# Performance work log

Measured on AMD Instinct MI355X. Metric: run time of the kernel, lower is better.

Reference implementation:

```python
import jax, jax.numpy as jnp
import numpy as np

B, S, D = 16, 512, 768      # batch, max_n_words, context_dim (input_size)
E, R = 128, 2048            # entities per doc, candidate relations per doc
H = 768                     # config.hidden_size
H2 = H // 2                 # 384
OUT = 2                     # binary relation classes


def _linear_params(k, fan_in, fan_out):
    k1, k2 = jax.random.split(k)
    bound = 1.0 / np.sqrt(fan_in)
    W = jax.random.uniform(k1, (fan_in, fan_out), minval=-bound, maxval=bound, dtype=jnp.float32)
    b = jax.random.uniform(k2, (fan_out,), minval=-bound, maxval=bound, dtype=jnp.float32)
    return W, b


def setup_inputs() -> dict:
    key = jax.random.key(0)
    ks = jax.random.split(key, 16)
    hW1, hb1 = _linear_params(ks[0], 2 * D, H)
    hW2, hb2 = _linear_params(ks[1], H, H2)
    tW1, tb1 = _linear_params(ks[2], 2 * D, H)
    tW2, tb2 = _linear_params(ks[3], H, H2)
    bnd = 1.0 / np.sqrt(H2)
    bil_w = jax.random.uniform(ks[4], (OUT, H2, H2), minval=-bnd, maxval=bnd, dtype=jnp.float32)
    lW, lb = _linear_params(ks[5], 2 * H2, OUT)
    emb = jax.random.normal(ks[6], (3, D), dtype=jnp.float32)  # entity_emb
    hidden_states = jax.random.normal(ks[7], (B, S, D), dtype=jnp.float32)
    ent_start = jax.random.randint(ks[8], (B, E), 0, S)
    ent_label = jax.random.randint(ks[9], (B, E), 0, 3)
    rel_head = jax.random.randint(ks[10], (B, R), 0, E)
    rel_tail = jax.random.randint(ks[11], (B, R), 0, E)
    rel_label = jax.random.randint(ks[12], (B, R), 0, 2)
    return dict(hidden_states=hidden_states, emb=emb,
                hW1=hW1, hb1=hb1, hW2=hW2, hb2=hb2,
                tW1=tW1, tb1=tb1, tW2=tW2, tb2=tb2,
                bil_w=bil_w, lW=lW, lb=lb,
                ent_start=ent_start, ent_label=ent_label,
                rel_head=rel_head, rel_tail=rel_tail, rel_label=rel_label)


def reference(hidden_states, emb, hW1, hb1, hW2, hb2, tW1, tb1, tW2, tb2,
              bil_w, lW, lb, ent_start, ent_label, rel_head, rel_tail, rel_label):
    def tower(rel_idx, W1, b1, W2, b2):
        start = jnp.take_along_axis(ent_start, rel_idx, axis=1)              # [B,R]
        lab = jnp.take_along_axis(ent_label, rel_idx, axis=1)                # [B,R]
        hid = jnp.take_along_axis(hidden_states, start[..., None], axis=1)   # [B,R,D]
        rep = jnp.concatenate([hid, emb[lab]], axis=-1)                      # [B,R,2D]
        h = jax.nn.relu(rep @ W1 + b1)                                       # [B,R,H]
        return jax.nn.relu(h @ W2 + b2)                                      # [B,R,H2]

    heads = tower(rel_head, hW1, hb1, hW2, hb2)
    tails = tower(rel_tail, tW1, tb1, tW2, tb2)
    # Biaffine: bilinear (no bias) + linear over concat
    logits = (jnp.einsum('bri,oij,brj->bro', heads, bil_w, tails)
              + jnp.concatenate([heads, tails], axis=-1) @ lW + lb)          # [B,R,2]
    logp = jax.nn.log_softmax(logits, axis=-1)
    loss = -jnp.mean(jnp.take_along_axis(logp, rel_label[..., None], axis=-1))
    return loss, logits
```

## Files before the change

### kernel.cpp

```cpp
#include <hip/hip_runtime.h>
#include <hip/hip_bf16.h>
#include <cstdint>

typedef unsigned short ushort_t;
typedef __bf16 bf16x8 __attribute__((ext_vector_type(8)));
typedef float f32x4 __attribute__((ext_vector_type(4)));

#define B_   16
#define S_   512
#define D_   768
#define E_   128
#define R_   2048
#define NREL 32768

__device__ inline ushort_t f2b(float f) {
    uint32_t u = __builtin_bit_cast(uint32_t, f);
    uint32_t r = (u + 0x7fffu + ((u >> 16) & 1u)) >> 16;
    return (ushort_t)r;
}
__device__ inline float b2f(ushort_t u) {
    uint32_t v = ((uint32_t)u) << 16;
    return __builtin_bit_cast(float, v);
}
__device__ inline float bl(uint32_t u) {
    uint32_t v = u << 16;
    return __builtin_bit_cast(float, v);
}
__device__ inline float bh(uint32_t u) {
    uint32_t v = u & 0xffff0000u;
    return __builtin_bit_cast(float, v);
}

__global__ __launch_bounds__(256) void prep_kernel(
    const float* __restrict__ hidden, const float* __restrict__ lW,
    const int* __restrict__ ent_start,
    ushort_t* __restrict__ repE, ushort_t* __restrict__ BmatT,
    ushort_t* __restrict__ lWtT, float* __restrict__ out)
{
    int idx = blockIdx.x * 256 + threadIdx.x;
    if (idx == 0) out[0] = 0.0f;
    if (idx < 393216) {
        int row = idx / 192, q = idx - row * 192;
        int c = q * 4;
        int b = row >> 7;
        int st = ent_start[row];
        const float* srcp = hidden + ((size_t)(b * S_ + st) * D_ + c);
        float4 v = *reinterpret_cast<const float4*>(srcp);
        uint32_t lo = (uint32_t)f2b(v.x) | ((uint32_t)f2b(v.y) << 16);
        uint32_t hi = (uint32_t)f2b(v.z) | ((uint32_t)f2b(v.w) << 16);
        uint2 pk; pk.x = lo; pk.y = hi;
        *reinterpret_cast<uint2*>(repE + (size_t)idx * 4) = pk;
        return;
    }
    int i2 = idx - 393216;
    if (i2 < 768) {
        int o = i2 / 384, kk = i2 - o * 384;
        BmatT[(768 + o) * 384 + kk] = f2b(lW[kk * 2 + o]);
        return;
    }
    i2 -= 768;
    if (i2 < 768) {
        int o = i2 / 384, ii = i2 - o * 384;
        lWtT[o * 384 + ii] = f2b(lW[(384 + ii) * 2 + o]);
    }
}

__global__ __launch_bounds__(256) void transpose_w(
    const float* __restrict__ hW1, const float* __restrict__ tW1,
    const float* __restrict__ hW2, const float* __restrict__ tW2,
    const float* __restrict__ bil, const float* __restrict__ emb,
    const float* __restrict__ hb1, const float* __restrict__ tb1,
    ushort_t* __restrict__ hW1T, ushort_t* __restrict__ tW1T,
    ushort_t* __restrict__ hW2T, ushort_t* __restrict__ tW2T,
    ushort_t* __restrict__ BmatT,
    float* __restrict__ biasEh, float* __restrict__ biasEt)
{
    __shared__ float smem[1056];
    int z = blockIdx.z;
    if (z >= 6) {
        if (blockIdx.y || blockIdx.x >= 12) return;
        const float* W1 = (z == 6) ? hW1 : tW1;
        const float* b1 = (z == 6) ? hb1 : tb1;
        float* dstB     = (z == 6) ? biasEh : biasEt;
        int c64 = threadIdx.x & 63, kc = threadIdx.x >> 6;
        int col = blockIdx.x * 64 + c64;
        float a0 = 0.f, a1 = 0.f, a2 = 0.f;
        const float* wp = W1 + (size_t)(768 + kc * 192) * 768 + col;
        const float* e0 = emb + kc * 192;
        for (int k = 0; k < 192; ++k) {
            float w = wp[(size_t)k * 768];
            a0 += e0[k] * w;
            a1 += e0[768 + k] * w;
            a2 += e0[1536 + k] * w;
        }
        smem[(kc * 3 + 0) * 64 + c64] = a0;
        smem[(kc * 3 + 1) * 64 + c64] = a1;
        smem[(kc * 3 + 2) * 64 + c64] = a2;
        __syncthreads();
        if (kc == 0) {
            float bv = b1[col];
#pragma unroll
            for (int l = 0; l < 3; ++l) {
                float s = smem[l * 64 + c64] + smem[(3 + l) * 64 + c64]
                        + smem[(6 + l) * 64 + c64] + smem[(9 + l) * 64 + c64];
                dstB[l * 768 + col] = bv + s;
            }
        }
        return;
    }
    const float* src; ushort_t* dst; int Rr, Cc;
    switch (z) {
        case 0:  src = hW1;          dst = hW1T;           Rr = 768; Cc = 768; break;
        case 1:  src = tW1;          dst = tW1T;           Rr = 768; Cc = 768; break;
        case 2:  src = hW2;          dst = hW2T;           Rr = 768; Cc = 384; break;
        case 3:  src = tW2;          dst = tW2T;           Rr = 768; Cc = 384; break;
        case 4:  src = bil;          dst = BmatT;          Rr = 384; Cc = 384; break;
        default: src = bil + 147456; dst = BmatT + 147456; Rr = 384; Cc = 384; break;
    }
    int tR = blockIdx.x * 32, tC = blockIdx.y * 32;
    if (tR >= Rr || tC >= Cc) return;
    int tx = threadIdx.x & 31, ty = threadIdx.x >> 5;
#pragma unroll
    for (int r = 0; r < 4; ++r)
        smem[(ty + r * 8) * 33 + tx] = src[(size_t)(tR + ty + r * 8) * Cc + tC + tx];
    __syncthreads();
#pragma unroll
    for (int r = 0; r < 4; ++r)
        dst[(size_t)(tC + ty + r * 8) * Rr + tR + tx] = f2b(smem[tx * 33 + ty + r * 8]);
}

__global__ __launch_bounds__(256) void gemm_lds(
    const ushort_t* __restrict__ A0, const ushort_t* __restrict__ A1,
    const ushort_t* __restrict__ Bt0, const ushort_t* __restrict__ Bt1,
    const float* __restrict__ bias0, const float* __restrict__ bias1,
    void* __restrict__ out0, void* __restrict__ out1,
    const int* __restrict__ lab,
    int M, int N0, int N1, int K, int doRelu, int f32o0, int f32o1)
{
    __shared__ ushort_t As[64 * 32];
    __shared__ ushort_t Bs[64 * 32];
    int N = blockIdx.z ? N1 : N0;
    int tileN = blockIdx.y * 64;
    if (tileN >= N) return;
    const ushort_t* A   = blockIdx.z ? A1 : A0;
    const ushort_t* Bt  = blockIdx.z ? Bt1 : Bt0;
    const float*   bias = blockIdx.z ? bias1 : bias0;
    int           f32o  = blockIdx.z ? f32o1 : f32o0;
    ushort_t*      outH = (ushort_t*)(blockIdx.z ? out1 : out0);
    float*         outF = (float*)(blockIdx.z ? out1 : out0);

    int t = threadIdx.x;
    int lane = t & 63, wave = t >> 6;
    int tileM = blockIdx.x * 64;
    int wm = (wave >> 1) * 32, wn = (wave & 1) * 32;
    int l15 = lane & 15, quad = lane >> 4;

    const ushort_t* gA = A  + (size_t)tileM * K;
    const ushort_t* gB = Bt + (size_t)tileN * K;

    int srow = t >> 2, sc8 = (t & 3) << 3;

    f32x4 acc[2][2];
#pragma unroll
    for (int a = 0; a < 2; ++a)
#pragma unroll
        for (int b = 0; b < 2; ++b) {
            acc[a][b][0] = 0.f; acc[a][b][1] = 0.f;
            acc[a][b][2] = 0.f; acc[a][b][3] = 0.f;
        }

    for (int k0 = 0; k0 < K; k0 += 32) {
        __builtin_amdgcn_global_load_lds(
            (const __attribute__((address_space(1))) void*)(gA + (size_t)srow * K + k0 + sc8),
            (__attribute__((address_space(3))) void*)(As + t * 8), 16, 0, 0);
        __builtin_amdgcn_global_load_lds(
            (const __attribute__((address_space(1))) void*)(gB + (size_t)srow * K + k0 + sc8),
            (__attribute__((address_space(3))) void*)(Bs + t * 8), 16, 0, 0);
        __syncthreads();
        bf16x8 af[2], bfr[2];
#pragma unroll
        for (int mi = 0; mi < 2; ++mi)
            af[mi] = *reinterpret_cast<const bf16x8*>(As + (wm + mi * 16 + l15) * 32 + quad * 8);
#pragma unroll
        for (int ni = 0; ni < 2; ++ni)
            bfr[ni] = *reinterpret_cast<const bf16x8*>(Bs + (wn + ni * 16 + l15) * 32 + quad * 8);
#pragma unroll
        for (int mi = 0; mi < 2; ++mi)
#pragma unroll
            for (int ni = 0; ni < 2; ++ni)
                acc[mi][ni] = __builtin_amdgcn_mfma_f32_16x16x32_bf16(af[mi], bfr[ni], acc[mi][ni], 0, 0, 0);
        __syncthreads();
    }

#pragma unroll
    for (int mi = 0; mi < 2; ++mi) {
        int gr = tileM + wm + mi * 16 + quad * 4;
        int lb4[4];
        if (lab) {
#pragma unroll
            for (int r = 0; r < 4; ++r) lb4[r] = lab[gr + r];
        }
#pragma unroll
        for (int ni = 0; ni < 2; ++ni) {
            int gc = tileN + wn + ni * 16 + l15;
            if (gc < N) {
#pragma unroll
                for (int r = 0; r < 4; ++r) {
                    float bb = lab ? bias[(size_t)lb4[r] * N + gc]
                                   : (bias ? bias[gc] : 0.0f);
                    float v = acc[mi][ni][r] + bb;
                    if (doRelu) v = fmaxf(v, 0.0f);
                    if (f32o) outF[(size_t)(gr + r) * N + gc] = v;
                    else      outH[(size_t)(gr + r) * N + gc] = f2b(v);
                }
            }
        }
    }
}

__global__ __launch_bounds__(256) void rel_kernel(
    const ushort_t* __restrict__ Uext, const ushort_t* __restrict__ tailsE,
    const float* __restrict__ tLin, const float* __restrict__ lb,
    const int* __restrict__ rel_head, const int* __restrict__ rel_tail,
    const int* __restrict__ rel_label, float* __restrict__ out)
{
    __shared__ float wsum[4];
    int lane = threadIdx.x & 63, wave = threadIdx.x >> 6;
    float lb0 = lb[0], lb1 = lb[1];
    float lossAcc = 0.0f;
    int base = (blockIdx.x * 4 + wave) * 8;

    for (int q = 0; q < 8; ++q) {
        int rel = base + q;
        int b = rel >> 11;
        int h = rel_head[rel], t = rel_tail[rel], lab = rel_label[rel];
        const uint32_t* uh = reinterpret_cast<const uint32_t*>(Uext + (size_t)(b * E_ + h) * 770);
        const uint32_t* tv = reinterpret_cast<const uint32_t*>(tailsE + (size_t)(b * E_ + t) * 384);

        float a0 = 0.f, a1 = 0.f;
#pragma unroll
        for (int j = 0; j < 3; ++j) {
            int i = lane + 64 * j;
            uint32_t tu = tv[i];
            uint32_t u0 = uh[i], u1 = uh[192 + i];
            float tl = bl(tu), th = bh(tu);
            a0 += tl * bl(u0) + th * bh(u0);
            a1 += tl * bl(u1) + th * bh(u1);
        }
#pragma unroll
        for (int d = 1; d < 64; d <<= 1) {
            a0 += __shfl_xor(a0, d);
            a1 += __shfl_xor(a1, d);
        }
        const ushort_t* uhs = reinterpret_cast<const ushort_t*>(uh);
        float2 tp = reinterpret_cast<const float2*>(tLin)[b * E_ + t];
        float l0v = a0 + tp.x + b2f(uhs[768]) + lb0;
        float l1v = a1 + tp.y + b2f(uhs[769]) + lb1;
        if (lane == 0) {
            out[1 + 2 * rel]     = l0v;
            out[1 + 2 * rel + 1] = l1v;
        }
        float m = fmaxf(l0v, l1v);
        float lse = m + logf(expf(l0v - m) + expf(l1v - m));
        lossAcc += lse - (lab ? l1v : l0v);
    }
    if (lane == 0) wsum[wave] = lossAcc;
    __syncthreads();
    if (threadIdx.x == 0) {
        float s = wsum[0] + wsum[1] + wsum[2] + wsum[3];
        atomicAdd(out, s * (1.0f / 32768.0f));
    }
}

extern "C" void kernel_launch(void* const* d_in, const int* in_sizes, int n_in,
                              void* d_out, int out_size, void* d_ws, size_t ws_size,
                              hipStream_t stream)
{
    const float* hidden = (const float*)d_in[0];
    const float* emb    = (const float*)d_in[1];
    const float* hW1    = (const float*)d_in[2];
    const float* hb1    = (const float*)d_in[3];
    const float* hW2    = (const float*)d_in[4];
    const float* hb2    = (const float*)d_in[5];
    const float* tW1    = (const float*)d_in[6];
    const float* tb1    = (const float*)d_in[7];
    const float* tW2    = (const float*)d_in[8];
    const float* tb2    = (const float*)d_in[9];
    const float* bil    = (const float*)d_in[10];
    const float* lW     = (const float*)d_in[11];
    const float* lb     = (const float*)d_in[12];
    const int* ent_start = (const int*)d_in[13];
    const int* ent_label = (const int*)d_in[14];
    const int* rel_head  = (const int*)d_in[15];
    const int* rel_tail  = (const int*)d_in[16];
    const int* rel_label = (const int*)d_in[17];
    float* out = (float*)d_out;

    char* ws = (char*)d_ws;
    ushort_t* repE   = (ushort_t*)(ws + 0);
    ushort_t* hW1T   = (ushort_t*)(ws + 3145728);
    ushort_t* tW1T   = (ushort_t*)(ws + 4325376);
    ushort_t* hW2T   = (ushort_t*)(ws + 5505024);
    ushort_t* tW2T   = (ushort_t*)(ws + 6094848);
    ushort_t* BmatT  = (ushort_t*)(ws + 6684672);
    ushort_t* lWtT   = (ushort_t*)(ws + 7276032);
    float*    biasEh = (float*)   (ws + 7277568);
    float*    biasEt = (float*)   (ws + 7286784);
    float*    tLin   = (float*)   (ws + 7296000);
    ushort_t* h1     = (ushort_t*)(ws + 7312384);
    ushort_t* t1     = (ushort_t*)(ws + 10458112);
    ushort_t* headsE = (ushort_t*)(ws + 13603840);
    ushort_t* tailsE = (ushort_t*)(ws + 15176704);
    ushort_t* Uext   = (ushort_t*)(ws + 16749568);

    prep_kernel<<<1542, 256, 0, stream>>>(
        hidden, lW, ent_start, repE, BmatT, lWtT, out);

    transpose_w<<<dim3(24, 24, 8), 256, 0, stream>>>(
        hW1, tW1, hW2, tW2, bil, emb, hb1, tb1,
        hW1T, tW1T, hW2T, tW2T, BmatT, biasEh, biasEt);

    gemm_lds<<<dim3(32, 12, 2), 256, 0, stream>>>(
        repE, repE, hW1T, tW1T, biasEh, biasEt, h1, t1, ent_label,
        2048, 768, 768, 768, 1, 0, 0);

    gemm_lds<<<dim3(32, 6, 2), 256, 0, stream>>>(
        h1, t1, hW2T, tW2T, hb2, tb2, headsE, tailsE, nullptr,
        2048, 384, 384, 768, 1, 0, 0);

    gemm_lds<<<dim3(32, 13, 2), 256, 0, stream>>>(
        headsE, tailsE, BmatT, lWtT, nullptr, nullptr, Uext, tLin, nullptr,
        2048, 770, 2, 384, 0, 0, 1);

    rel_kernel<<<1024, 256, 0, stream>>>(
        Uext, tailsE, tLin, lb, rel_head, rel_tail, rel_label, out);
}
```

Before: 188.7 us.

## Double-buffer GEMM LDS tiles with swizzle and split bias-table K loop

The GEMM kernel now keeps two LDS buffers, issuing the next K-tile's global-to-LDS loads before the MFMAs on the current tile, with one barrier per iteration instead of two. An XOR swizzle is applied to the LDS layout to reduce bank conflicts on fragment reads. The entity-embedding bias precompute is split across 16 K-chunks per column block and combined with atomicAdd into buffers zeroed in prep_kernel, raising parallelism of a previously serial 192-step loop. It relies on the async LDS load completing before the next barrier, and atomic accumulation makes bias summation order nondeterministic.

```diff
diff --git a/kernel.cpp b/kernel.cpp
--- a/kernel.cpp
+++ b/kernel.cpp
@@ -35,7 +35,8 @@
     const float* __restrict__ hidden, const float* __restrict__ lW,
     const int* __restrict__ ent_start,
     ushort_t* __restrict__ repE, ushort_t* __restrict__ BmatT,
-    ushort_t* __restrict__ lWtT, float* __restrict__ out)
+    ushort_t* __restrict__ lWtT, float* __restrict__ biasEh,
+    float* __restrict__ out)
 {
     int idx = blockIdx.x * 256 + threadIdx.x;
     if (idx == 0) out[0] = 0.0f;
@@ -62,7 +63,10 @@
     if (i2 < 768) {
         int o = i2 / 384, ii = i2 - o * 384;
         lWtT[o * 384 + ii] = f2b(lW[(384 + ii) * 2 + o]);
-    }
+        return;
+    }
+    i2 -= 768;
+    if (i2 < 4608) biasEh[i2] = 0.0f;
 }
 
 __global__ __launch_bounds__(256) void transpose_w(
@@ -78,32 +82,35 @@
     __shared__ float smem[1056];
     int z = blockIdx.z;
     if (z >= 6) {
-        if (blockIdx.y || blockIdx.x >= 12) return;
+        int bx = blockIdx.x, by = blockIdx.y;
+        if (bx >= 12 || by >= 16) return;
         const float* W1 = (z == 6) ? hW1 : tW1;
         const float* b1 = (z == 6) ? hb1 : tb1;
         float* dstB     = (z == 6) ? biasEh : biasEt;
-        int c64 = threadIdx.x & 63, kc = threadIdx.x >> 6;
-        int col = blockIdx.x * 64 + c64;
+        int c64 = threadIdx.x & 63, kg = threadIdx.x >> 6;
+        int col = bx * 64 + c64;
+        int k0r = by * 48 + kg * 12;
+        const float* wp = W1 + (size_t)(768 + k0r) * 768 + col;
+        const float* e0 = emb + k0r;
         float a0 = 0.f, a1 = 0.f, a2 = 0.f;
-        const float* wp = W1 + (size_t)(768 + kc * 192) * 768 + col;
-        const float* e0 = emb + kc * 192;
-        for (int k = 0; k < 192; ++k) {
+#pragma unroll
+        for (int k = 0; k < 12; ++k) {
             float w = wp[(size_t)k * 768];
             a0 += e0[k] * w;
             a1 += e0[768 + k] * w;
             a2 += e0[1536 + k] * w;
         }
-        smem[(kc * 3 + 0) * 64 + c64] = a0;
-        smem[(kc * 3 + 1) * 64 + c64] = a1;
-        smem[(kc * 3 + 2) * 64 + c64] = a2;
+        smem[(kg * 3 + 0) * 64 + c64] = a0;
+        smem[(kg * 3 + 1) * 64 + c64] = a1;
+        smem[(kg * 3 + 2) * 64 + c64] = a2;
         __syncthreads();
-        if (kc == 0) {
-            float bv = b1[col];
+        if (kg == 0) {
+            float bv = (by == 0) ? b1[col] : 0.0f;
 #pragma unroll
             for (int l = 0; l < 3; ++l) {
                 float s = smem[l * 64 + c64] + smem[(3 + l) * 64 + c64]
                         + smem[(6 + l) * 64 + c64] + smem[(9 + l) * 64 + c64];
-                dstB[l * 768 + col] = bv + s;
+                atomicAdd(&dstB[l * 768 + col], bv + s);
             }
         }
         return;
@@ -137,8 +144,8 @@
     const int* __restrict__ lab,
     int M, int N0, int N1, int K, int doRelu, int f32o0, int f32o1)
 {
-    __shared__ ushort_t As[64 * 32];
-    __shared__ ushort_t Bs[64 * 32];
+    __shared__ ushort_t As[2][2048];
+    __shared__ ushort_t Bs[2][2048];
     int N = blockIdx.z ? N1 : N0;
     int tileN = blockIdx.y * 64;
     if (tileN >= N) return;
@@ -155,10 +162,18 @@
     int wm = (wave >> 1) * 32, wn = (wave & 1) * 32;
     int l15 = lane & 15, quad = lane >> 4;
 
-    const ushort_t* gA = A  + (size_t)tileM * K;
-    const ushort_t* gB = Bt + (size_t)tileN * K;
-
-    int srow = t >> 2, sc8 = (t & 3) << 3;
+    int srow = t >> 2;
+    int sgl  = (((t & 3) ^ ((t >> 3) & 3)) << 3);
+    const ushort_t* pA = A  + (size_t)(tileM + srow) * K + sgl;
+    const ushort_t* pB = Bt + (size_t)(tileN + srow) * K + sgl;
+    int ldst = t * 8;
+
+    int rA0 = wm + l15,      rA1 = wm + 16 + l15;
+    int rB0 = wn + l15,      rB1 = wn + 16 + l15;
+    int offA0 = rA0 * 32 + ((quad ^ ((rA0 >> 1) & 3)) << 3);
+    int offA1 = rA1 * 32 + ((quad ^ ((rA1 >> 1) & 3)) << 3);
+    int offB0 = rB0 * 32 + ((quad ^ ((rB0 >> 1) & 3)) << 3);
+    int offB1 = rB1 * 32 + ((quad ^ ((rB1 >> 1) & 3)) << 3);
 
     f32x4 acc[2][2];
 #pragma unroll
@@ -169,26 +184,34 @@
             acc[a][b][2] = 0.f; acc[a][b][3] = 0.f;
         }
 
-    for (int k0 = 0; k0 < K; k0 += 32) {
-        __builtin_amdgcn_global_load_lds(
-            (const __attribute__((address_space(1))) void*)(gA + (size_t)srow * K + k0 + sc8),
-            (__attribute__((address_space(3))) void*)(As + t * 8), 16, 0, 0);
-        __builtin_amdgcn_global_load_lds(
-            (const __attribute__((address_space(1))) void*)(gB + (size_t)srow * K + k0 + sc8),
-            (__attribute__((address_space(3))) void*)(Bs + t * 8), 16, 0, 0);
-        __syncthreads();
-        bf16x8 af[2], bfr[2];
-#pragma unroll
-        for (int mi = 0; mi < 2; ++mi)
-            af[mi] = *reinterpret_cast<const bf16x8*>(As + (wm + mi * 16 + l15) * 32 + quad * 8);
-#pragma unroll
-        for (int ni = 0; ni < 2; ++ni)
-            bfr[ni] = *reinterpret_cast<const bf16x8*>(Bs + (wn + ni * 16 + l15) * 32 + quad * 8);
-#pragma unroll
-        for (int mi = 0; mi < 2; ++mi)
-#pragma unroll
-            for (int ni = 0; ni < 2; ++ni)
-                acc[mi][ni] = __builtin_amdgcn_mfma_f32_16x16x32_bf16(af[mi], bfr[ni], acc[mi][ni], 0, 0, 0);
+    __builtin_amdgcn_global_load_lds(
+        (const __attribute__((address_space(1))) void*)pA,
+        (__attribute__((address_space(3))) void*)(&As[0][ldst]), 16, 0, 0);
+    __builtin_amdgcn_global_load_lds(
+        (const __attribute__((address_space(1))) void*)pB,
+        (__attribute__((address_space(3))) void*)(&Bs[0][ldst]), 16, 0, 0);
+    __syncthreads();
+
+    int nk = K >> 5;
+    for (int kt = 0; kt < nk; ++kt) {
+        int cur = kt & 1;
+        if (kt + 1 < nk) {
+            int ko = (kt + 1) << 5;
+            __builtin_amdgcn_global_load_lds(
+                (const __attribute__((address_space(1))) void*)(pA + ko),
+                (__attribute__((address_space(3))) void*)(&As[cur ^ 1][ldst]), 16, 0, 0);
+            __builtin_amdgcn_global_load_lds(
+                (const __attribute__((address_space(1))) void*)(pB + ko),
+                (__attribute__((address_space(3))) void*)(&Bs[cur ^ 1][ldst]), 16, 0, 0);
+        }
+        bf16x8 af0 = *reinterpret_cast<const bf16x8*>(&As[cur][offA0]);
+        bf16x8 af1 = *reinterpret_cast<const bf16x8*>(&As[cur][offA1]);
+        bf16x8 bf0 = *reinterpret_cast<const bf16x8*>(&Bs[cur][offB0]);
+        bf16x8 bf1 = *reinterpret_cast<const bf16x8*>(&Bs[cur][offB1]);
+        acc[0][0] = __builtin_amdgcn_mfma_f32_16x16x32_bf16(af0, bf0, acc[0][0], 0, 0, 0);
+        acc[0][1] = __builtin_amdgcn_mfma_f32_16x16x32_bf16(af0, bf1, acc[0][1], 0, 0, 0);
+        acc[1][0] = __builtin_amdgcn_mfma_f32_16x16x32_bf16(af1, bf0, acc[1][0], 0, 0, 0);
+        acc[1][1] = __builtin_amdgcn_mfma_f32_16x16x32_bf16(af1, bf1, acc[1][1], 0, 0, 0);
         __syncthreads();
     }
 
@@ -313,8 +336,8 @@
     ushort_t* tailsE = (ushort_t*)(ws + 15176704);
     ushort_t* Uext   = (ushort_t*)(ws + 16749568);
 
-    prep_kernel<<<1542, 256, 0, stream>>>(
-        hidden, lW, ent_start, repE, BmatT, lWtT, out);
+    prep_kernel<<<1560, 256, 0, stream>>>(
+        hidden, lW, ent_start, repE, BmatT, lWtT, biasEh, out);
 
     transpose_w<<<dim3(24, 24, 8), 256, 0, stream>>>(
         hW1, tW1, hW2, tW2, bil, emb, hb1, tb1,
```

Result: faster. 175.3 us (-7.1%).

## Double-buffer GEMM K loop with swizzled LDS and fuse prep kernels

Applied to the files above, without the earlier changes.

The GEMM main loop now uses a K-step of 64, with two LDS buffers and an XOR-swizzled layout. The next tile's global-to-LDS loads are issued before the current tile's MFMAs, which halves the barriers per K and aims to hide load latency and bank conflicts. The two preprocessing kernels (gather/convert and weight transpose plus embedding-bias compute) are merged into one flat-grid launch, and the bias computation is vectorized with float4 and split finer. This adds LDS use (32KB per block) and index complexity, which may lower occupancy.

```diff
diff --git a/kernel.cpp b/kernel.cpp
--- a/kernel.cpp
+++ b/kernel.cpp
@@ -31,103 +31,126 @@
     return __builtin_bit_cast(float, v);
 }
 
-__global__ __launch_bounds__(256) void prep_kernel(
-    const float* __restrict__ hidden, const float* __restrict__ lW,
-    const int* __restrict__ ent_start,
-    ushort_t* __restrict__ repE, ushort_t* __restrict__ BmatT,
-    ushort_t* __restrict__ lWtT, float* __restrict__ out)
-{
-    int idx = blockIdx.x * 256 + threadIdx.x;
-    if (idx == 0) out[0] = 0.0f;
-    if (idx < 393216) {
-        int row = idx / 192, q = idx - row * 192;
-        int c = q * 4;
-        int b = row >> 7;
-        int st = ent_start[row];
-        const float* srcp = hidden + ((size_t)(b * S_ + st) * D_ + c);
-        float4 v = *reinterpret_cast<const float4*>(srcp);
-        uint32_t lo = (uint32_t)f2b(v.x) | ((uint32_t)f2b(v.y) << 16);
-        uint32_t hi = (uint32_t)f2b(v.z) | ((uint32_t)f2b(v.w) << 16);
-        uint2 pk; pk.x = lo; pk.y = hi;
-        *reinterpret_cast<uint2*>(repE + (size_t)idx * 4) = pk;
-        return;
-    }
-    int i2 = idx - 393216;
-    if (i2 < 768) {
-        int o = i2 / 384, kk = i2 - o * 384;
-        BmatT[(768 + o) * 384 + kk] = f2b(lW[kk * 2 + o]);
-        return;
-    }
-    i2 -= 768;
-    if (i2 < 768) {
-        int o = i2 / 384, ii = i2 - o * 384;
-        lWtT[o * 384 + ii] = f2b(lW[(384 + ii) * 2 + o]);
-    }
-}
-
-__global__ __launch_bounds__(256) void transpose_w(
+#define NB_BIAS 24
+#define NB_PREP 1542
+
+__global__ __launch_bounds__(256) void prep_fused(
+    const float* __restrict__ hidden, const float* __restrict__ emb,
+    const float* __restrict__ lW,
     const float* __restrict__ hW1, const float* __restrict__ tW1,
     const float* __restrict__ hW2, const float* __restrict__ tW2,
-    const float* __restrict__ bil, const float* __restrict__ emb,
+    const float* __restrict__ bil,
     const float* __restrict__ hb1, const float* __restrict__ tb1,
+    const int* __restrict__ ent_start,
+    ushort_t* __restrict__ repE,
     ushort_t* __restrict__ hW1T, ushort_t* __restrict__ tW1T,
     ushort_t* __restrict__ hW2T, ushort_t* __restrict__ tW2T,
-    ushort_t* __restrict__ BmatT,
-    float* __restrict__ biasEh, float* __restrict__ biasEt)
+    ushort_t* __restrict__ BmatT, ushort_t* __restrict__ lWtT,
+    float* __restrict__ biasEh, float* __restrict__ biasEt,
+    float* __restrict__ out)
 {
-    __shared__ float smem[1056];
-    int z = blockIdx.z;
-    if (z >= 6) {
-        if (blockIdx.y || blockIdx.x >= 12) return;
-        const float* W1 = (z == 6) ? hW1 : tW1;
-        const float* b1 = (z == 6) ? hb1 : tb1;
-        float* dstB     = (z == 6) ? biasEh : biasEt;
-        int c64 = threadIdx.x & 63, kc = threadIdx.x >> 6;
-        int col = blockIdx.x * 64 + c64;
-        float a0 = 0.f, a1 = 0.f, a2 = 0.f;
-        const float* wp = W1 + (size_t)(768 + kc * 192) * 768 + col;
-        const float* e0 = emb + kc * 192;
-        for (int k = 0; k < 192; ++k) {
-            float w = wp[(size_t)k * 768];
-            a0 += e0[k] * w;
-            a1 += e0[768 + k] * w;
-            a2 += e0[1536 + k] * w;
-        }
-        smem[(kc * 3 + 0) * 64 + c64] = a0;
-        smem[(kc * 3 + 1) * 64 + c64] = a1;
-        smem[(kc * 3 + 2) * 64 + c64] = a2;
+    __shared__ float smem[3072];
+    int bid = blockIdx.x;
+    int tid = threadIdx.x;
+
+    if (bid < NB_BIAS) {
+        int tower = bid / 12, cb = bid - tower * 12;
+        const float* W1 = tower ? tW1 : hW1;
+        const float* b1 = tower ? tb1 : hb1;
+        float* dstB     = tower ? biasEt : biasEh;
+        int c4 = (tid & 15) * 4;
+        int kg = tid >> 4;
+        int col0 = cb * 64;
+        const float* wp = W1 + (size_t)(768 + kg * 48) * 768 + col0 + c4;
+        const float* ep = emb + kg * 48;
+        float a0x = 0.f, a0y = 0.f, a0z = 0.f, a0w = 0.f;
+        float a1x = 0.f, a1y = 0.f, a1z = 0.f, a1w = 0.f;
+        float a2x = 0.f, a2y = 0.f, a2z = 0.f, a2w = 0.f;
+#pragma unroll 8
+        for (int k = 0; k < 48; ++k) {
+            float4 w = *reinterpret_cast<const float4*>(wp + (size_t)k * 768);
+            float e0 = ep[k], e1 = ep[768 + k], e2 = ep[1536 + k];
+            a0x += e0 * w.x; a0y += e0 * w.y; a0z += e0 * w.z; a0w += e0 * w.w;
+            a1x += e1 * w.x; a1y += e1 * w.y; a1z += e1 * w.z; a1w += e1 * w.w;
+            a2x += e2 * w.x; a2y += e2 * w.y; a2z += e2 * w.z; a2w += e2 * w.w;
+        }
+        smem[kg * 192 +   0 + c4 + 0] = a0x;
+        smem[kg * 192 +   0 + c4 + 1] = a0y;
+        smem[kg * 192 +   0 + c4 + 2] = a0z;
+        smem[kg * 192 +   0 + c4 + 3] = a0w;
+        smem[kg * 192 +  64 + c4 + 0] = a1x;
+        smem[kg * 192 +  64 + c4 + 1] = a1y;
+        smem[kg * 192 +  64 + c4 + 2] = a1z;
+        smem[kg * 192 +  64 + c4 + 3] = a1w;
+        smem[kg * 192 + 128 + c4 + 0] = a2x;
+        smem[kg * 192 + 128 + c4 + 1] = a2y;
+        smem[kg * 192 + 128 + c4 + 2] = a2z;
+        smem[kg * 192 + 128 + c4 + 3] = a2w;
         __syncthreads();
-        if (kc == 0) {
-            float bv = b1[col];
-#pragma unroll
-            for (int l = 0; l < 3; ++l) {
-                float s = smem[l * 64 + c64] + smem[(3 + l) * 64 + c64]
-                        + smem[(6 + l) * 64 + c64] + smem[(9 + l) * 64 + c64];
-                dstB[l * 768 + col] = bv + s;
-            }
+        if (tid < 192) {
+            int l = tid >> 6, c = tid & 63;
+            float s = 0.f;
+#pragma unroll
+            for (int g = 0; g < 16; ++g) s += smem[g * 192 + l * 64 + c];
+            dstB[l * 768 + col0 + c] = b1[col0 + c] + s;
         }
         return;
     }
-    const float* src; ushort_t* dst; int Rr, Cc;
-    switch (z) {
-        case 0:  src = hW1;          dst = hW1T;           Rr = 768; Cc = 768; break;
-        case 1:  src = tW1;          dst = tW1T;           Rr = 768; Cc = 768; break;
-        case 2:  src = hW2;          dst = hW2T;           Rr = 768; Cc = 384; break;
-        case 3:  src = tW2;          dst = tW2T;           Rr = 768; Cc = 384; break;
-        case 4:  src = bil;          dst = BmatT;          Rr = 384; Cc = 384; break;
-        default: src = bil + 147456; dst = BmatT + 147456; Rr = 384; Cc = 384; break;
-    }
-    int tR = blockIdx.x * 32, tC = blockIdx.y * 32;
-    if (tR >= Rr || tC >= Cc) return;
-    int tx = threadIdx.x & 31, ty = threadIdx.x >> 5;
-#pragma unroll
-    for (int r = 0; r < 4; ++r)
-        smem[(ty + r * 8) * 33 + tx] = src[(size_t)(tR + ty + r * 8) * Cc + tC + tx];
+
+    int pb = bid - NB_BIAS;
+    if (pb < NB_PREP) {
+        int idx = pb * 256 + tid;
+        if (idx == 0) out[0] = 0.0f;
+        if (idx < 393216) {
+            int row = idx / 192, q = idx - row * 192;
+            int c = q * 4;
+            int b = row >> 7;
+            int st = ent_start[row];
+            const float* srcp = hidden + ((size_t)(b * S_ + st) * D_ + c);
+            float4 v = *reinterpret_cast<const float4*>(srcp);
+            uint32_t lo = (uint32_t)f2b(v.x) | ((uint32_t)f2b(v.y) << 16);
+            uint32_t hi = (uint32_t)f2b(v.z) | ((uint32_t)f2b(v.w) << 16);
+            uint2 pk; pk.x = lo; pk.y = hi;
+            *reinterpret_cast<uint2*>(repE + (size_t)idx * 4) = pk;
+            return;
+        }
+        int i2 = idx - 393216;
+        if (i2 < 768) {
+            int o = i2 / 384, kk = i2 - o * 384;
+            BmatT[(768 + o) * 384 + kk] = f2b(lW[kk * 2 + o]);
+            return;
+        }
+        i2 -= 768;
+        if (i2 < 768) {
+            int o = i2 / 384, ii = i2 - o * 384;
+            lWtT[o * 384 + ii] = f2b(lW[(384 + ii) * 2 + o]);
+        }
+        return;
+    }
+
+    int r = pb - NB_PREP;
+    const float* src; ushort_t* dst; int Rr, Cc, xs;
+    if (r < 576)        { src = hW1;          dst = hW1T;  Rr = 768; Cc = 768; xs = 24; }
+    else if (r < 1152)  { r -= 576;  src = tW1;          dst = tW1T;  Rr = 768; Cc = 768; xs = 24; }
+    else if (r < 1440)  { r -= 1152; src = hW2;          dst = hW2T;  Rr = 768; Cc = 384; xs = 24; }
+    else if (r < 1728)  { r -= 1440; src = tW2;          dst = tW2T;  Rr = 768; Cc = 384; xs = 24; }
+    else if (r < 1872)  { r -= 1728; src = bil;          dst = BmatT; Rr = 384; Cc = 384; xs = 12; }
+    else                { r -= 1872; src = bil + 147456; dst = BmatT + 147456; Rr = 384; Cc = 384; xs = 12; }
+    int bx = r % xs, by = r / xs;
+    int tR = bx * 32, tC = by * 32;
+    int tx = tid & 31, ty = tid >> 5;
+#pragma unroll
+    for (int rr = 0; rr < 4; ++rr)
+        smem[(ty + rr * 8) * 33 + tx] = src[(size_t)(tR + ty + rr * 8) * Cc + tC + tx];
     __syncthreads();
 #pragma unroll
-    for (int r = 0; r < 4; ++r)
-        dst[(size_t)(tC + ty + r * 8) * Rr + tR + tx] = f2b(smem[tx * 33 + ty + r * 8]);
-}
+    for (int rr = 0; rr < 4; ++rr)
+        dst[(size_t)(tC + ty + rr * 8) * Rr + tR + tx] = f2b(smem[tx * 33 + ty + rr * 8]);
+}
+
+#define GLL16(src, dst) __builtin_amdgcn_global_load_lds( \
+    (const __attribute__((address_space(1))) void*)(src), \
+    (__attribute__((address_space(3))) void*)(dst), 16, 0, 0)
 
 __global__ __launch_bounds__(256) void gemm_lds(
     const ushort_t* __restrict__ A0, const ushort_t* __restrict__ A1,
@@ -137,8 +160,8 @@
     const int* __restrict__ lab,
     int M, int N0, int N1, int K, int doRelu, int f32o0, int f32o1)
 {
-    __shared__ ushort_t As[64 * 32];
-    __shared__ ushort_t Bs[64 * 32];
+    __shared__ ushort_t As[2][4096];
+    __shared__ ushort_t Bs[2][4096];
     int N = blockIdx.z ? N1 : N0;
     int tileN = blockIdx.y * 64;
     if (tileN >= N) return;
@@ -155,10 +178,30 @@
     int wm = (wave >> 1) * 32, wn = (wave & 1) * 32;
     int l15 = lane & 15, quad = lane >> 4;
 
-    const ushort_t* gA = A  + (size_t)tileM * K;
-    const ushort_t* gB = Bt + (size_t)tileN * K;
-
-    int srow = t >> 2, sc8 = (t & 3) << 3;
+    int grow  = wave * 16 + (lane >> 3);
+    int gseg8 = ((lane & 7) ^ (lane >> 3)) << 3;
+    const ushort_t* pA0 = A  + (size_t)(tileM + grow) * K + gseg8;
+    const ushort_t* pA1 = A  + (size_t)(tileM + grow + 8) * K + gseg8;
+    const ushort_t* pB0 = Bt + (size_t)(tileN + grow) * K + gseg8;
+    const ushort_t* pB1 = Bt + (size_t)(tileN + grow + 8) * K + gseg8;
+    int ld0 = wave * 1024 + lane * 8;
+    int ld1 = ld0 + 512;
+
+    int offA[2][2], offB[2][2];
+#pragma unroll
+    for (int mi = 0; mi < 2; ++mi) {
+        int rw = wm + mi * 16 + l15;
+#pragma unroll
+        for (int ks = 0; ks < 2; ++ks)
+            offA[mi][ks] = rw * 64 + (((ks * 4 + quad) ^ (rw & 7)) << 3);
+    }
+#pragma unroll
+    for (int ni = 0; ni < 2; ++ni) {
+        int rw = wn + ni * 16 + l15;
+#pragma unroll
+        for (int ks = 0; ks < 2; ++ks)
+            offB[ni][ks] = rw * 64 + (((ks * 4 + quad) ^ (rw & 7)) << 3);
+    }
 
     f32x4 acc[2][2];
 #pragma unroll
@@ -169,26 +212,36 @@
             acc[a][b][2] = 0.f; acc[a][b][3] = 0.f;
         }
 
-    for (int k0 = 0; k0 < K; k0 += 32) {
-        __builtin_amdgcn_global_load_lds(
-            (const __attribute__((address_space(1))) void*)(gA + (size_t)srow * K + k0 + sc8),
-            (__attribute__((address_space(3))) void*)(As + t * 8), 16, 0, 0);
-        __builtin_amdgcn_global_load_lds(
-            (const __attribute__((address_space(1))) void*)(gB + (size_t)srow * K + k0 + sc8),
-            (__attribute__((address_space(3))) void*)(Bs + t * 8), 16, 0, 0);
-        __syncthreads();
-        bf16x8 af[2], bfr[2];
-#pragma unroll
-        for (int mi = 0; mi < 2; ++mi)
-            af[mi] = *reinterpret_cast<const bf16x8*>(As + (wm + mi * 16 + l15) * 32 + quad * 8);
-#pragma unroll
-        for (int ni = 0; ni < 2; ++ni)
-            bfr[ni] = *reinterpret_cast<const bf16x8*>(Bs + (wn + ni * 16 + l15) * 32 + quad * 8);
-#pragma unroll
-        for (int mi = 0; mi < 2; ++mi)
-#pragma unroll
-            for (int ni = 0; ni < 2; ++ni)
-                acc[mi][ni] = __builtin_amdgcn_mfma_f32_16x16x32_bf16(af[mi], bfr[ni], acc[mi][ni], 0, 0, 0);
+    GLL16(pA0, &As[0][ld0]); GLL16(pA1, &As[0][ld1]);
+    GLL16(pB0, &Bs[0][ld0]); GLL16(pB1, &Bs[0][ld1]);
+    __syncthreads();
+
+    int nk = K >> 6;
+    for (int kt = 0; kt < nk; ++kt) {
+        int cur = kt & 1;
+        if (kt + 1 < nk) {
+            int ko = (kt + 1) << 6;
+            GLL16(pA0 + ko, &As[cur ^ 1][ld0]);
+            GLL16(pA1 + ko, &As[cur ^ 1][ld1]);
+            GLL16(pB0 + ko, &Bs[cur ^ 1][ld0]);
+            GLL16(pB1 + ko, &Bs[cur ^ 1][ld1]);
+        }
+        bf16x8 a0k0 = *reinterpret_cast<const bf16x8*>(&As[cur][offA[0][0]]);
+        bf16x8 a1k0 = *reinterpret_cast<const bf16x8*>(&As[cur][offA[1][0]]);
+        bf16x8 b0k0 = *reinterpret_cast<const bf16x8*>(&Bs[cur][offB[0][0]]);
+        bf16x8 b1k0 = *reinterpret_cast<const bf16x8*>(&Bs[cur][offB[1][0]]);
+        bf16x8 a0k1 = *reinterpret_cast<const bf16x8*>(&As[cur][offA[0][1]]);
+        bf16x8 a1k1 = *reinterpret_cast<const bf16x8*>(&As[cur][offA[1][1]]);
+        bf16x8 b0k1 = *reinterpret_cast<const bf16x8*>(&Bs[cur][offB[0][1]]);
+        bf16x8 b1k1 = *reinterpret_cast<const bf16x8*>(&Bs[cur][offB[1][1]]);
+        acc[0][0] = __builtin_amdgcn_mfma_f32_16x16x32_bf16(a0k0, b0k0, acc[0][0], 0, 0, 0);
+        acc[0][1] = __builtin_amdgcn_mfma_f32_16x16x32_bf16(a0k0, b1k0, acc[0][1], 0, 0, 0);
+        acc[1][0] = __builtin_amdgcn_mfma_f32_16x16x32_bf16(a1k0, b0k0, acc[1][0], 0, 0, 0);
+        acc[1][1] = __builtin_amdgcn_mfma_f32_16x16x32_bf16(a1k0, b1k0, acc[1][1], 0, 0, 0);
+        acc[0][0] = __builtin_amdgcn_mfma_f32_16x16x32_bf16(a0k1, b0k1, acc[0][0], 0, 0, 0);
+        acc[0][1] = __builtin_amdgcn_mfma_f32_16x16x32_bf16(a0k1, b1k1, acc[0][1], 0, 0, 0);
+        acc[1][0] = __builtin_amdgcn_mfma_f32_16x16x32_bf16(a1k1, b0k1, acc[1][0], 0, 0, 0);
+        acc[1][1] = __builtin_amdgcn_mfma_f32_16x16x32_bf16(a1k1, b1k1, acc[1][1], 0, 0, 0);
         __syncthreads();
     }
 
@@ -313,12 +366,9 @@
     ushort_t* tailsE = (ushort_t*)(ws + 15176704);
     ushort_t* Uext   = (ushort_t*)(ws + 16749568);
 
-    prep_kernel<<<1542, 256, 0, stream>>>(
-        hidden, lW, ent_start, repE, BmatT, lWtT, out);
-
-    transpose_w<<<dim3(24, 24, 8), 256, 0, stream>>>(
-        hW1, tW1, hW2, tW2, bil, emb, hb1, tb1,
-        hW1T, tW1T, hW2T, tW2T, BmatT, biasEh, biasEt);
+    prep_fused<<<3582, 256, 0, stream>>>(
+        hidden, emb, lW, hW1, tW1, hW2, tW2, bil, hb1, tb1, ent_start,
+        repE, hW1T, tW1T, hW2T, tW2T, BmatT, lWtT, biasEh, biasEt, out);
 
     gemm_lds<<<dim3(32, 12, 2), 256, 0, stream>>>(
         repE, repE, hW1T, tW1T, biasEh, biasEt, h1, t1, ent_label,
```

Measured after the change: 173.6 us. -8.0%, faster.
